# Performance work log

Hardware: AMD Instinct MI355X
Metric: run time of the kernel (lower is better)

## Reference

```python
import jax, jax.numpy as jnp
import numpy as np

N_CONTEXT = 256  # teacher-forced prefix length (n_context)
N_INPUTS = 2
HID = 16         # LSTM hidden_size
PROJ = 2         # LSTM proj_size


def setup_inputs() -> dict:
    key = jax.random.key(0)
    ks = jax.random.split(key, 6)
    B, T = 4096, 1024
    s = 1.0 / np.sqrt(HID)  # torch LSTM init range
    return {
        "u_train": jax.random.normal(ks[0], (B, T, N_INPUTS + PROJ), jnp.float32),
        "w_ih": jax.random.uniform(ks[1], (4 * HID, N_INPUTS), jnp.float32, -s, s),
        "w_hh": jax.random.uniform(ks[2], (4 * HID, PROJ), jnp.float32, -s, s),
        "b_ih": jax.random.uniform(ks[3], (4 * HID,), jnp.float32, -s, s),
        "b_hh": jax.random.uniform(ks[4], (4 * HID,), jnp.float32, -s, s),
        "w_hr": jax.random.uniform(ks[5], (PROJ, HID), jnp.float32, -s, s),
    }


def _cell(x, h, c, w_ih, w_hh, b, w_hr):
    # PyTorch LSTM gate order: i, f, g, o; projected output h = (o*tanh(c)) @ w_hr.T
    gates = x @ w_ih.T + h @ w_hh.T + b  # [B, 4*HID]
    i, f, g, o = jnp.split(gates, 4, axis=-1)
    c_new = jax.nn.sigmoid(f) * c + jax.nn.sigmoid(i) * jnp.tanh(g)
    h_new = (jax.nn.sigmoid(o) * jnp.tanh(c_new)) @ w_hr.T  # [B, PROJ]
    return h_new, c_new


def reference(u_train, w_ih, w_hh, b_ih, b_hh, w_hr):
    B = u_train.shape[0]
    u = u_train[..., :N_INPUTS]   # [B, T, 2] exogenous inputs
    y = u_train[..., N_INPUTS:]
    b = b_ih + b_hh

    xs_est = (jnp.swapaxes(u[:, :N_CONTEXT], 0, 1),  # [nstep, B, 2]
              jnp.swapaxes(y[:, :N_CONTEXT], 0, 1))
    c0 = jnp.zeros((B, HID), u_train.dtype)

    def est_step(c, xy):
        x_t, y_t = xy
        h_new, c_new = _cell(x_t, y_t, c, w_ih, w_hh, b, w_hr)
        return c_new, h_new

    cn, h_est = jax.lax.scan(est_step, c0, xs_est)  # h_est: [nstep, B, 2]
    hn = h_est[-1]

    # ---- predict_state: free-running LSTM from (hn, cn) ----
    def pred_step(carry, x_t):
        h, c = carry
        h_new, c_new = _cell(x_t, h, c, w_ih, w_hh, b, w_hr)
        return (h_new, c_new), h_new

    _, h_pred = jax.lax.scan(pred_step, (hn, cn), jnp.swapaxes(u[:, N_CONTEXT:], 0, 1))

    return jnp.concatenate([jnp.swapaxes(h_est, 0, 1), jnp.swapaxes(h_pred, 0, 1)], axis=1)
```

## Files before the change

kernel.cpp:

```cpp
#include <hip/hip_runtime.h>

#define N_CTX  256
#define T_LEN  1024
#define N_SEQ  4096
#define CHUNK  16
#define NCHUNK (T_LEN / CHUNK)
#define CTXCK  (N_CTX / CHUNK)

typedef float v2f __attribute__((ext_vector_type(2)));

__device__ __forceinline__ float fexp2(float x){ return __builtin_amdgcn_exp2f(x); }
__device__ __forceinline__ float frcp (float x){ return __builtin_amdgcn_rcpf(x); }
__device__ __forceinline__ v2f pk_fma(v2f a, v2f b, v2f c){ return __builtin_elementwise_fma(a, b, c); }

#define L1C 1.4426950408889634f
#define L2C 2.8853901631790583f
#define WCLAMP 100.0f

template<int CTRL>
__device__ __forceinline__ v2f dpp_add2(v2f x){
    int y0 = __builtin_amdgcn_mov_dpp(__float_as_int(x.x), CTRL, 0xf, 0xf, true);
    int y1 = __builtin_amdgcn_mov_dpp(__float_as_int(x.y), CTRL, 0xf, 0xf, true);
    v2f y = { __int_as_float(y0), __int_as_float(y1) };
    return x + y;
}
__device__ __forceinline__ v2f red16_2(v2f x){
    x = dpp_add2<0xB1>(x);
    x = dpp_add2<0x4E>(x);
    x = dpp_add2<0x124>(x);
    x = dpp_add2<0x128>(x);
    return x;
}

struct LaneW {
    v2f wi0_if, wi1_if, wi0_go, wi1_go;
    v2f wh0_if, wh1_if, wh0_go, wh1_go;
    v2f bs_if, bs_go;
    v2f whr;
};

struct ChunkX {
    v2f   xif[CHUNK];
    v2f   xgo[CHUNK];
    float y0[CHUNK], y1[CHUNK];
};

__device__ __forceinline__ void load_chunk(float4* b, const float4* __restrict__ up, int base){
#pragma unroll
    for (int i = 0; i < CHUNK; ++i) b[i] = up[base + i];
}

template<bool TEACHER>
__device__ __forceinline__ void transform_chunk(ChunkX& X, const float4* raw, const LaneW& L){
#pragma unroll
    for (int i = 0; i < CHUNK; ++i) {
        const float4 x = raw[i];
        v2f xx = {x.x, x.x}, xy = {x.y, x.y};
        X.xif[i] = pk_fma(xy, L.wi1_if, pk_fma(xx, L.wi0_if, L.bs_if));
        X.xgo[i] = pk_fma(xy, L.wi1_go, pk_fma(xx, L.wi0_go, L.bs_go));
        if (TEACHER) { X.y0[i] = x.z; X.y1[i] = x.w; }
        else         { X.y0[i] = 0.f; X.y1[i] = 0.f; }
    }
}

template<bool TEACHER>
__device__ __forceinline__ void lstm_step(v2f xif, v2f xgo, float y0, float y1,
                                          const LaneW& L, float& c, v2f& rh)
{
    const float h0 = TEACHER ? y0 : rh.x;
    const float h1 = TEACHER ? y1 : rh.y;
    v2f hh0 = {h0, h0}, hh1 = {h1, h1};
    v2f gif = pk_fma(hh1, L.wh1_if, pk_fma(hh0, L.wh0_if, xif));
    v2f ggo = pk_fma(hh1, L.wh1_go, pk_fma(hh0, L.wh0_go, xgo));
    const float u  = fexp2(gif.x);
    const float ef = fexp2(gif.y);
    const float v  = fexp2(ggo.x);
    const float eo = fexp2(ggo.y);
    const float A   = (1.0f + u) * (v + 1.0f);
    const float B   = 1.0f + ef;
    const float t   = (v - 1.0f) * B;
    const float num = fmaf(c, A, t);
    c = num * frcp(A * B);
    const float w = fexp2(fminf(L2C * c, WCLAMP));
    const float s = (w - 1.0f) * frcp((1.0f + eo) * (w + 1.0f));
    v2f ss = {s, s};
    rh = red16_2(ss * L.whr);
}

template<bool TEACHER>
__device__ __forceinline__ void chain_chunk(const ChunkX& X, int baseT, const LaneW& L,
                                            float& c, v2f& rh,
                                            float2* __restrict__ op2, int j)
{
    v2f cap = rh;
#pragma unroll
    for (int i = 0; i < CHUNK; ++i) {
        lstm_step<TEACHER>(X.xif[i], X.xgo[i], X.y0[i], X.y1[i], L, c, rh);
        cap = (j == i) ? rh : cap;
    }
    float2 o; o.x = cap.x; o.y = cap.y;
    op2[baseT + j] = o;
}

__global__ __launch_bounds__(256, 1) void openlstm_kernel(
    const float* __restrict__ u,
    const float* __restrict__ w_ih,
    const float* __restrict__ w_hh,
    const float* __restrict__ b_ih,
    const float* __restrict__ b_hh,
    const float* __restrict__ w_hr,
    float* __restrict__ out)
{
    const int tid = blockIdx.x * blockDim.x + threadIdx.x;
    const int seq = tid >> 4;
    const int j   = tid & 15;

    LaneW L;
    {
        const int ri = j, rf = 16 + j, rg = 32 + j, ro = 48 + j;
        const v2f sif = {-L1C, -L1C};
        const v2f sgo = { L2C, -L1C};
        L.wi0_if = sif * (v2f){w_ih[ri*2+0], w_ih[rf*2+0]};
        L.wi1_if = sif * (v2f){w_ih[ri*2+1], w_ih[rf*2+1]};
        L.wi0_go = sgo * (v2f){w_ih[rg*2+0], w_ih[ro*2+0]};
        L.wi1_go = sgo * (v2f){w_ih[rg*2+1], w_ih[ro*2+1]};
        L.wh0_if = sif * (v2f){w_hh[ri*2+0], w_hh[rf*2+0]};
        L.wh1_if = sif * (v2f){w_hh[ri*2+1], w_hh[rf*2+1]};
        L.wh0_go = sgo * (v2f){w_hh[rg*2+0], w_hh[ro*2+0]};
        L.wh1_go = sgo * (v2f){w_hh[rg*2+1], w_hh[ro*2+1]};
        L.bs_if  = sif * (v2f){b_ih[ri] + b_hh[ri], b_ih[rf] + b_hh[rf]};
        L.bs_go  = sgo * (v2f){b_ih[rg] + b_hh[rg], b_ih[ro] + b_hh[ro]};
        L.whr    = (v2f){w_hr[j], w_hr[16 + j]};
    }

    const float4* __restrict__ up = (const float4*)u + (size_t)seq * T_LEN;
    float2* __restrict__ op2 = (float2*)out + (size_t)seq * T_LEN;

    float c = 0.0f;
    v2f rh = {0.0f, 0.0f};
    float4 rawA[CHUNK], rawB[CHUNK];

    load_chunk(rawA, up, 0);
    load_chunk(rawB, up, CHUNK);

#pragma unroll 1
    for (int ck = 0; ck < CTXCK; ck += 2) {
        {
            ChunkX XA;
            transform_chunk<true>(XA, rawA, L);
            load_chunk(rawA, up, (ck + 2) * CHUNK);
            chain_chunk<true>(XA, ck * CHUNK, L, c, rh, op2, j);
        }
        {
            ChunkX XB;
            transform_chunk<true>(XB, rawB, L);
            load_chunk(rawB, up, (ck + 3) * CHUNK);
            chain_chunk<true>(XB, (ck + 1) * CHUNK, L, c, rh, op2, j);
        }
    }

#pragma unroll 1
    for (int ck = CTXCK; ck < NCHUNK; ck += 2) {
        const int lA = (ck + 2 < NCHUNK) ? (ck + 2) : (NCHUNK - 1);
        const int lB = (ck + 3 < NCHUNK) ? (ck + 3) : (NCHUNK - 1);
        {
            ChunkX XA;
            transform_chunk<false>(XA, rawA, L);
            load_chunk(rawA, up, lA * CHUNK);
            chain_chunk<false>(XA, ck * CHUNK, L, c, rh, op2, j);
        }
        {
            ChunkX XB;
            transform_chunk<false>(XB, rawB, L);
            load_chunk(rawB, up, lB * CHUNK);
            chain_chunk<false>(XB, (ck + 1) * CHUNK, L, c, rh, op2, j);
        }
    }
}

extern "C" void kernel_launch(void* const* d_in, const int* in_sizes, int n_in,
                              void* d_out, int out_size, void* d_ws, size_t ws_size,
                              hipStream_t stream) {
    const float* u    = (const float*)d_in[0];
    const float* w_ih = (const float*)d_in[1];
    const float* w_hh = (const float*)d_in[2];
    const float* b_ih = (const float*)d_in[3];
    const float* b_hh = (const float*)d_in[4];
    const float* w_hr = (const float*)d_in[5];
    float* out = (float*)d_out;

    const int threads = 256;
    const int blocks  = (N_SEQ * 16) / threads;
    hipLaunchKernelGGL(openlstm_kernel, dim3(blocks), dim3(threads), 0, stream,
                       u, w_ih, w_hh, b_ih, b_hh, w_hr, out);
}
```

Measured before the change: 217.7 us.

## Break teacher-forced phase into gate precompute, linear cell scan, and output pass

In the teacher-forced estimation phase the gates depend only on known inputs, so the cell update becomes an affine recurrence c = P*c + Q. The change computes all gates and the P, Q coefficients for a chunk in parallel, runs a short serial FMA chain over c, and then evaluates tanh, the projection and the DPP reductions independently per step. This takes the exp, rcp and reduction latency out of the serial dependency chain for the first 256 steps, at the cost of more live registers per chunk (P, Q, EO, CA arrays). The loads are now issued after each chunk's compute instead of between transform and chain.

```diff
diff --git a/kernel.cpp b/kernel.cpp
--- a/kernel.cpp
+++ b/kernel.cpp
@@ -39,18 +39,58 @@
     v2f whr;
 };
 
+__device__ __forceinline__ void load_chunk(float4* b, const float4* __restrict__ up, int base){
+#pragma unroll
+    for (int i = 0; i < CHUNK; ++i) b[i] = up[base + i];
+}
+
+__device__ __forceinline__ void est_chunk(const float4* raw, int baseT, const LaneW& L,
+                                          float& c, v2f& rh,
+                                          float2* __restrict__ op2, int j)
+{
+    float P[CHUNK], Q[CHUNK], EO[CHUNK];
+#pragma unroll
+    for (int i = 0; i < CHUNK; ++i) {
+        const float4 x = raw[i];
+        v2f xx = {x.x, x.x}, xy = {x.y, x.y};
+        v2f y0 = {x.z, x.z}, y1 = {x.w, x.w};
+        v2f gif = pk_fma(y1, L.wh1_if, pk_fma(y0, L.wh0_if,
+                  pk_fma(xy, L.wi1_if, pk_fma(xx, L.wi0_if, L.bs_if))));
+        v2f ggo = pk_fma(y1, L.wh1_go, pk_fma(y0, L.wh0_go,
+                  pk_fma(xy, L.wi1_go, pk_fma(xx, L.wi0_go, L.bs_go))));
+        const float u  = fexp2(gif.x);
+        const float ef = fexp2(gif.y);
+        const float v  = fexp2(ggo.x);
+        const float eo = fexp2(ggo.y);
+        const float A  = (1.0f + u) * (v + 1.0f);
+        const float B  = 1.0f + ef;
+        const float r  = frcp(A * B);
+        P[i]  = A * r;
+        Q[i]  = (v - 1.0f) * B * r;
+        EO[i] = 1.0f + eo;
+    }
+    float CA[CHUNK];
+#pragma unroll
+    for (int i = 0; i < CHUNK; ++i) { c = fmaf(P[i], c, Q[i]); CA[i] = c; }
+    v2f cap = rh;
+#pragma unroll
+    for (int i = 0; i < CHUNK; ++i) {
+        const float w = fexp2(fminf(L2C * CA[i], WCLAMP));
+        const float s = (w - 1.0f) * frcp(EO[i] * (w + 1.0f));
+        v2f ss = {s, s};
+        v2f hv = red16_2(ss * L.whr);
+        cap = (j == i) ? hv : cap;
+        if (i == CHUNK - 1) rh = hv;
+    }
+    float2 o; o.x = cap.x; o.y = cap.y;
+    op2[baseT + j] = o;
+}
+
 struct ChunkX {
-    v2f   xif[CHUNK];
-    v2f   xgo[CHUNK];
-    float y0[CHUNK], y1[CHUNK];
+    v2f xif[CHUNK];
+    v2f xgo[CHUNK];
 };
 
-__device__ __forceinline__ void load_chunk(float4* b, const float4* __restrict__ up, int base){
-#pragma unroll
-    for (int i = 0; i < CHUNK; ++i) b[i] = up[base + i];
-}
-
-template<bool TEACHER>
 __device__ __forceinline__ void transform_chunk(ChunkX& X, const float4* raw, const LaneW& L){
 #pragma unroll
     for (int i = 0; i < CHUNK; ++i) {
@@ -58,18 +98,13 @@
         v2f xx = {x.x, x.x}, xy = {x.y, x.y};
         X.xif[i] = pk_fma(xy, L.wi1_if, pk_fma(xx, L.wi0_if, L.bs_if));
         X.xgo[i] = pk_fma(xy, L.wi1_go, pk_fma(xx, L.wi0_go, L.bs_go));
-        if (TEACHER) { X.y0[i] = x.z; X.y1[i] = x.w; }
-        else         { X.y0[i] = 0.f; X.y1[i] = 0.f; }
-    }
-}
-
-template<bool TEACHER>
-__device__ __forceinline__ void lstm_step(v2f xif, v2f xgo, float y0, float y1,
-                                          const LaneW& L, float& c, v2f& rh)
-{
-    const float h0 = TEACHER ? y0 : rh.x;
-    const float h1 = TEACHER ? y1 : rh.y;
-    v2f hh0 = {h0, h0}, hh1 = {h1, h1};
+    }
+}
+
+__device__ __forceinline__ void pred_step(v2f xif, v2f xgo, const LaneW& L,
+                                          float& c, v2f& rh)
+{
+    v2f hh0 = {rh.x, rh.x}, hh1 = {rh.y, rh.y};
     v2f gif = pk_fma(hh1, L.wh1_if, pk_fma(hh0, L.wh0_if, xif));
     v2f ggo = pk_fma(hh1, L.wh1_go, pk_fma(hh0, L.wh0_go, xgo));
     const float u  = fexp2(gif.x);
@@ -81,21 +116,21 @@
     const float t   = (v - 1.0f) * B;
     const float num = fmaf(c, A, t);
     c = num * frcp(A * B);
+    const float eop = 1.0f + eo;
     const float w = fexp2(fminf(L2C * c, WCLAMP));
-    const float s = (w - 1.0f) * frcp((1.0f + eo) * (w + 1.0f));
+    const float s = (w - 1.0f) * frcp(eop * (w + 1.0f));
     v2f ss = {s, s};
     rh = red16_2(ss * L.whr);
 }
 
-template<bool TEACHER>
-__device__ __forceinline__ void chain_chunk(const ChunkX& X, int baseT, const LaneW& L,
-                                            float& c, v2f& rh,
-                                            float2* __restrict__ op2, int j)
+__device__ __forceinline__ void pred_chunk(const ChunkX& X, int baseT, const LaneW& L,
+                                           float& c, v2f& rh,
+                                           float2* __restrict__ op2, int j)
 {
     v2f cap = rh;
 #pragma unroll
     for (int i = 0; i < CHUNK; ++i) {
-        lstm_step<TEACHER>(X.xif[i], X.xgo[i], X.y0[i], X.y1[i], L, c, rh);
+        pred_step(X.xif[i], X.xgo[i], L, c, rh);
         cap = (j == i) ? rh : cap;
     }
     float2 o; o.x = cap.x; o.y = cap.y;
@@ -145,18 +180,10 @@
 
 #pragma unroll 1
     for (int ck = 0; ck < CTXCK; ck += 2) {
-        {
-            ChunkX XA;
-            transform_chunk<true>(XA, rawA, L);
-            load_chunk(rawA, up, (ck + 2) * CHUNK);
-            chain_chunk<true>(XA, ck * CHUNK, L, c, rh, op2, j);
-        }
-        {
-            ChunkX XB;
-            transform_chunk<true>(XB, rawB, L);
-            load_chunk(rawB, up, (ck + 3) * CHUNK);
-            chain_chunk<true>(XB, (ck + 1) * CHUNK, L, c, rh, op2, j);
-        }
+        est_chunk(rawA, ck * CHUNK, L, c, rh, op2, j);
+        load_chunk(rawA, up, (ck + 2) * CHUNK);
+        est_chunk(rawB, (ck + 1) * CHUNK, L, c, rh, op2, j);
+        load_chunk(rawB, up, (ck + 3) * CHUNK);
     }
 
 #pragma unroll 1
@@ -165,15 +192,15 @@
         const int lB = (ck + 3 < NCHUNK) ? (ck + 3) : (NCHUNK - 1);
         {
             ChunkX XA;
-            transform_chunk<false>(XA, rawA, L);
+            transform_chunk(XA, rawA, L);
             load_chunk(rawA, up, lA * CHUNK);
-            chain_chunk<false>(XA, ck * CHUNK, L, c, rh, op2, j);
+            pred_chunk(XA, ck * CHUNK, L, c, rh, op2, j);
         }
         {
             ChunkX XB;
-            transform_chunk<false>(XB, rawB, L);
+            transform_chunk(XB, rawB, L);
             load_chunk(rawB, up, lB * CHUNK);
-            chain_chunk<false>(XB, (ck + 1) * CHUNK, L, c, rh, op2, j);
+            pred_chunk(XB, (ck + 1) * CHUNK, L, c, rh, op2, j);
         }
     }
 }
```

New measurement: 214.1 us. Within noise of the previous version (-1.7%).
